# Optimization experiments

Measured on AMD Instinct MI355X. Metric: run time of the kernel, lower is better.

The kernel has to match this reference:

```python
import jax, jax.numpy as jnp
import numpy as np

N = 20000; E = 640000
D_IN = 1000; E1 = 500; E2 = 500; E3 = 2000; NZ = 10; NC = 10


def setup_inputs() -> dict:
    keys = iter(jax.random.split(jax.random.key(0), 80))

    def nrm(shape, s=0.05):
        return jax.random.normal(next(keys), shape, jnp.float32) * s

    inp = {"x": jax.random.normal(next(keys), (N, D_IN), jnp.float32)}
    for nm in ["adj", "fadj", "f1", "f2"]:
        inp[nm + "_rows"] = jax.random.randint(next(keys), (E,), 0, N, jnp.int32)
        inp[nm + "_cols"] = jax.random.randint(next(keys), (E,), 0, N, jnp.int32)
        inp[nm + "_vals"] = jax.random.uniform(next(keys), (E,), jnp.float32)
    dims = [D_IN, E1, E2, E3, NZ]
    for br in ["fea", "topo"]:
        for i in range(4):
            inp[br + "_W" + str(i + 1)] = nrm((dims[i], dims[i + 1]))
    ae_shapes = {"e1": (D_IN, E1), "e2": (E1, E2), "e3": (E2, E3), "z1": (E3, NZ),
                 "z2": (NZ, NC), "d0": (NC, NZ), "d1": (NZ, 2000), "d2": (2000, 500),
                 "d3": (500, 500), "xb": (500, D_IN)}
    for nm, sh in ae_shapes.items():
        inp["ae_W" + nm] = nrm(sh)
        inp["ae_b" + nm] = jnp.zeros((sh[1],), jnp.float32)
    inp["mlpL_W"] = nrm((3000 + NZ, 5))
    inp["mlpL_b"] = jnp.zeros((5,), jnp.float32)
    return inp


def _bn(h):
    # BatchNorm1d(affine=False, track_running_stats=False): batch stats, biased var
    return (h - h.mean(0)) * jax.lax.rsqrt(h.var(0) + 1e-5)


def _branch(x, rows, cols, vals, Ws):
    # stacked GNNLayer: dense mm -> spmm(adj, support) -> leaky_relu(0.2) -> elu -> BN
    hs = []
    h = x
    for W in Ws:
        sup = h @ W                                            # [N, out]
        agg = jax.ops.segment_sum(vals[:, None] * sup[cols], rows, num_segments=N)
        h = _bn(jax.nn.elu(jax.nn.leaky_relu(agg, 0.2)))
        hs.append(h)
    return hs


def _forward(x,
             adj_rows, adj_cols, adj_vals,
             fadj_rows, fadj_cols, fadj_vals,
             f1_rows, f1_cols, f1_vals,
             f2_rows, f2_cols, f2_vals,
             fea_W1, fea_W2, fea_W3, fea_W4,
             topo_W1, topo_W2, topo_W3, topo_W4,
             ae_We1, ae_be1, ae_We2, ae_be2, ae_We3, ae_be3,
             ae_Wz1, ae_bz1, ae_Wz2, ae_bz2,
             ae_Wd0, ae_bd0, ae_Wd1, ae_bd1, ae_Wd2, ae_bd2, ae_Wd3, ae_bd3,
             ae_Wxb, ae_bxb, mlpL_W, mlpL_b):
    relu = jax.nn.relu
    # AE branch
    h1 = relu(x @ ae_We1 + ae_be1)
    h2 = relu(h1 @ ae_We2 + ae_be2)
    h3 = relu(h2 @ ae_We3 + ae_be3)
    z1 = h3 @ ae_Wz1 + ae_bz1
    z = z1 @ ae_Wz2 + ae_bz2
    d = relu(z @ ae_Wd0 + ae_bd0)
    d = relu(d @ ae_Wd1 + ae_bd1)
    d = relu(d @ ae_Wd2 + ae_bd2)
    d = relu(d @ ae_Wd3 + ae_bd3)
    x_bar = d @ ae_Wxb + ae_bxb
    feaWs = [fea_W1, fea_W2, fea_W3, fea_W4]
    topoWs = [topo_W1, topo_W2, topo_W3, topo_W4]
    fea_hs = _branch(x, fadj_rows, fadj_cols, fadj_vals, feaWs)
    fea_diff = _branch(x, f2_rows, f2_cols, f2_vals, feaWs)
    topo_hs = _branch(x, adj_rows, adj_cols, adj_vals, topoWs)
    topo_diff = _branch(x, f1_rows, f1_cols, f1_vals, topoWs)
    coms = jnp.concatenate(fea_hs, axis=1)                      # [N, 3000+NZ]
    u = jax.nn.softmax(jnp.tanh(coms @ mlpL_W + mlpL_b), axis=1)
    u = u / jnp.maximum(jnp.linalg.norm(u, axis=1, keepdims=True), 1e-12)  # F.normalize p=2
    z_out_fea = jnp.concatenate([u[:, i:i + 1] * fea_hs[i] for i in range(4)], axis=1)
    return (x_bar, z, fea_hs[3], topo_hs[3], fea_diff[3], topo_diff[3], z_out_fea)


def reference(x,
              adj_rows, adj_cols, adj_vals,
              fadj_rows, fadj_cols, fadj_vals,
              f1_rows, f1_cols, f1_vals,
              f2_rows, f2_cols, f2_vals,
              fea_W1, fea_W2, fea_W3, fea_W4,
              topo_W1, topo_W2, topo_W3, topo_W4,
              ae_We1, ae_be1, ae_We2, ae_be2, ae_We3, ae_be3,
              ae_Wz1, ae_bz1, ae_Wz2, ae_bz2,
              ae_Wd0, ae_bd0, ae_Wd1, ae_bd1, ae_Wd2, ae_bd2, ae_Wd3, ae_bd3,
              ae_Wxb, ae_bxb, mlpL_W, mlpL_b):
    return _forward(x, adj_rows, adj_cols, adj_vals, fadj_rows, fadj_cols, fadj_vals,
                    f1_rows, f1_cols, f1_vals, f2_rows, f2_cols, f2_vals,
                    fea_W1, fea_W2, fea_W3, fea_W4, topo_W1, topo_W2, topo_W3, topo_W4,
                    ae_We1, ae_be1, ae_We2, ae_be2, ae_We3, ae_be3,
                    ae_Wz1, ae_bz1, ae_Wz2, ae_bz2,
                    ae_Wd0, ae_bd0, ae_Wd1, ae_bd1, ae_Wd2, ae_bd2, ae_Wd3, ae_bd3,
                    ae_Wxb, ae_bxb, mlpL_W, mlpL_b)
```

## Files before the change

### kernel.cpp

```cpp
#include <hip/hip_runtime.h>
#include <cstdint>
#include <cstddef>

#define N_NODES 20000
#define N_EDGES 640000

typedef short short8 __attribute__((ext_vector_type(8)));
typedef float floatx4 __attribute__((ext_vector_type(4)));

__device__ __forceinline__ ushort f2bf(float f) {
    uint32_t u = __float_as_uint(f);
    uint32_t r = (u + 0x7fff + ((u >> 16) & 1)) >> 16;
    return (ushort)r;
}
__device__ __forceinline__ float bf2f(ushort u) {
    return __uint_as_float(((uint32_t)u) << 16);
}

__global__ __launch_bounds__(256) void zero_i32(int* __restrict__ p, int n) {
    int i = blockIdx.x * 256 + threadIdx.x;
    if (i < n) p[i] = 0;
}

__global__ __launch_bounds__(256) void transpose_w(const float* __restrict__ W,
                                                   ushort* __restrict__ Bt,
                                                   int K, int Nc, int Kp) {
    int idx = blockIdx.x * 256 + threadIdx.x;
    if (idx >= Nc * Kp) return;
    int n = idx / Kp, k = idx % Kp;
    Bt[idx] = (k < K) ? f2bf(W[(size_t)k * Nc + n]) : (ushort)0;
}

__global__ __launch_bounds__(256) void hist_kernel(const int* __restrict__ rows,
                                                   int* __restrict__ counts) {
    int e = blockIdx.x * 256 + threadIdx.x;
    if (e < N_EDGES) atomicAdd(&counts[rows[e]], 1);
}

__global__ __launch_bounds__(1024) void scan_kernel(const int* __restrict__ counts,
                                                    int* __restrict__ row_ptr) {
    __shared__ int part[1024];
    const int CH = 20;
    int tid = threadIdx.x;
    int t0 = tid * CH;
    int s = 0;
    for (int i = 0; i < CH; ++i) {
        int p = t0 + i;
        if (p < N_NODES) s += counts[p];
    }
    part[tid] = s;
    __syncthreads();
    for (int off = 1; off < 1024; off <<= 1) {
        int v = (tid >= off) ? part[tid - off] : 0;
        __syncthreads();
        if (tid >= off) part[tid] += v;
        __syncthreads();
    }
    int base = (tid == 0) ? 0 : part[tid - 1];
    for (int i = 0; i < CH; ++i) {
        int p = t0 + i;
        if (p < N_NODES) {
            row_ptr[p] = base;
            base += counts[p];
            if (p == N_NODES - 1) row_ptr[N_NODES] = base;
        }
    }
}

__global__ __launch_bounds__(256) void fill_kernel(const int* __restrict__ rows,
                                                   const int* __restrict__ cols,
                                                   const float* __restrict__ vals,
                                                   const int* __restrict__ row_ptr,
                                                   int* __restrict__ fillctr,
                                                   int* __restrict__ cols_s,
                                                   float* __restrict__ vals_s) {
    int e = blockIdx.x * 256 + threadIdx.x;
    if (e < N_EDGES) {
        int r = rows[e];
        int pos = atomicAdd(&fillctr[r], 1);
        int idx = row_ptr[r] + pos;
        cols_s[idx] = cols[e];
        vals_s[idx] = vals[e];
    }
}

template <int AMODE>
__global__ __launch_bounds__(256) void mfma_gemm(
    const float* __restrict__ A, const ushort* __restrict__ Ab,
    const ushort* __restrict__ Bt,
    const float* __restrict__ bias, float* __restrict__ Cf,
    ushort* __restrict__ Cb, int M, int K, int lda, int Nc, int ldc, int Kp,
    int act, int NX, int NY) {
    __shared__ __align__(16) ushort As[128][40];
    __shared__ __align__(16) ushort Bs[128][40];
    __shared__ __align__(16) ushort Al[(AMODE == 1) ? 128 : 1][40];

    int id = blockIdx.x;
    int r8 = id & 7, tt = id >> 3;
    int bx = tt % NX, qq = tt / NX;
    int by = r8 + 8 * qq;
    if (by >= NY) return;
    int row0 = by * 128, col0 = bx * 128;

    int tid = threadIdx.x;
    int wave = tid >> 6, lane = tid & 63;
    int wr = (wave >> 1) * 64, wc = (wave & 1) * 64;
    int m16 = lane & 15, quad = lane >> 4;

    floatx4 acc[4][4] = {};
    int KT = (K + 31) >> 5;
    bool k4 = (K & 3) == 0;

    int arf = tid >> 3, akq = (tid & 7) << 2;
    int arb = tid >> 2, akb = (tid & 3) << 3;
    int bn_ = tid >> 2, bch = (tid & 3) << 3;

    float4 avA[4], avB[4];
    uint4 abvA[2], abvB[2], bvA[2], bvB[2];

#define ISSUE_T(AV, ABV, BV, KTARG)                                          \
    do {                                                                     \
        int k0_ = (KTARG) << 5;                                              \
        if constexpr (AMODE == 2) {                                          \
            for (int p = 0; p < 2; ++p) {                                    \
                int grow = row0 + arb + p * 64;                              \
                int gk = k0_ + akb;                                          \
                uint4 z = {0u, 0u, 0u, 0u};                                  \
                if (grow < M) {                                              \
                    const ushort* ap = Ab + (size_t)grow * lda + gk;         \
                    if (gk + 7 < K) {                                        \
                        z = *(const uint4*)ap;                               \
                    } else {                                                 \
                        ushort tm[8] = {0, 0, 0, 0, 0, 0, 0, 0};             \
                        for (int j = 0; j < 8; ++j)                          \
                            if (gk + j < K) tm[j] = ap[j];                   \
                        z.x = (uint)tm[0] | ((uint)tm[1] << 16);             \
                        z.y = (uint)tm[2] | ((uint)tm[3] << 16);             \
                        z.z = (uint)tm[4] | ((uint)tm[5] << 16);             \
                        z.w = (uint)tm[6] | ((uint)tm[7] << 16);             \
                    }                                                        \
                }                                                            \
                ABV[p] = z;                                                  \
            }                                                                \
        } else {                                                             \
            for (int p = 0; p < 4; ++p) {                                    \
                int grow = row0 + arf + p * 32;                              \
                int gk = k0_ + akq;                                          \
                float4 v = {0.f, 0.f, 0.f, 0.f};                             \
                if (grow < M) {                                              \
                    const float* ap = A + (size_t)grow * lda + gk;           \
                    if (k4 && gk + 3 < K) {                                  \
                        v = *(const float4*)ap;                              \
                    } else {                                                 \
                        if (gk < K) v.x = ap[0];                             \
                        if (gk + 1 < K) v.y = ap[1];                         \
                        if (gk + 2 < K) v.z = ap[2];                         \
                        if (gk + 3 < K) v.w = ap[3];                         \
                    }                                                        \
                }                                                            \
                AV[p] = v;                                                   \
            }                                                                \
        }                                                                    \
        for (int p = 0; p < 2; ++p) {                                        \
            int gcol = col0 + bn_ + p * 64;                                  \
            uint4 z = {0u, 0u, 0u, 0u};                                      \
            if (gcol < Nc) z = *(const uint4*)&Bt[(size_t)gcol * Kp + k0_ + bch]; \
            BV[p] = z;                                                       \
        }                                                                    \
    } while (0)

#define WRITE_T(AV, ABV, BV)                                                 \
    do {                                                                     \
        if constexpr (AMODE == 2) {                                          \
            for (int p = 0; p < 2; ++p)                                      \
                *(uint4*)&As[arb + p * 64][akb] = ABV[p];                    \
        } else {                                                             \
            for (int p = 0; p < 4; ++p) {                                    \
                float4 v = AV[p];                                            \
                ushort4 hi;                                                  \
                hi.x = f2bf(v.x); hi.y = f2bf(v.y);                          \
                hi.z = f2bf(v.z); hi.w = f2bf(v.w);                          \
                *(ushort4*)&As[arf + p * 32][akq] = hi;                      \
                if constexpr (AMODE == 1) {                                  \
                    ushort4 lo;                                              \
                    lo.x = f2bf(v.x - bf2f(hi.x));                           \
                    lo.y = f2bf(v.y - bf2f(hi.y));                           \
                    lo.z = f2bf(v.z - bf2f(hi.z));                           \
                    lo.w = f2bf(v.w - bf2f(hi.w));                           \
                    *(ushort4*)&Al[arf + p * 32][akq] = lo;                  \
                }                                                            \
            }                                                                \
        }                                                                    \
        for (int p = 0; p < 2; ++p)                                          \
            *(uint4*)&Bs[bn_ + p * 64][bch] = BV[p];                         \
    } while (0)

    ISSUE_T(avA, abvA, bvA, 0);
    for (int kt = 0; kt < KT; ++kt) {
        if (kt) __syncthreads();
        if ((kt & 1) == 0) {
            WRITE_T(avA, abvA, bvA);
            if (kt + 1 < KT) ISSUE_T(avB, abvB, bvB, kt + 1);
        } else {
            WRITE_T(avB, abvB, bvB);
            if (kt + 1 < KT) ISSUE_T(avA, abvA, bvA, kt + 1);
        }
        __syncthreads();
        short8 a[4], b[4];
        int ko = quad * 8;
#pragma unroll
        for (int i = 0; i < 4; ++i) a[i] = *(short8*)&As[wr + i * 16 + m16][ko];
#pragma unroll
        for (int j = 0; j < 4; ++j) b[j] = *(short8*)&Bs[wc + j * 16 + m16][ko];
        if constexpr (AMODE == 1) {
            short8 al[4];
#pragma unroll
            for (int i = 0; i < 4; ++i) al[i] = *(short8*)&Al[wr + i * 16 + m16][ko];
#pragma unroll
            for (int i = 0; i < 4; ++i)
#pragma unroll
                for (int j = 0; j < 4; ++j)
                    acc[i][j] = __builtin_amdgcn_mfma_f32_16x16x32_bf16(
                        al[i], b[j], acc[i][j], 0, 0, 0);
        }
#pragma unroll
        for (int i = 0; i < 4; ++i)
#pragma unroll
            for (int j = 0; j < 4; ++j)
                acc[i][j] = __builtin_amdgcn_mfma_f32_16x16x32_bf16(
                    a[i], b[j], acc[i][j], 0, 0, 0);
    }
#undef ISSUE_T
#undef WRITE_T

#pragma unroll
    for (int i = 0; i < 4; ++i) {
        int rbase = row0 + wr + i * 16 + quad * 4;
#pragma unroll
        for (int j = 0; j < 4; ++j) {
            int gcol = col0 + wc + j * 16 + m16;
            if (gcol >= Nc) continue;
            float bv = bias ? bias[gcol] : 0.f;
#pragma unroll
            for (int r = 0; r < 4; ++r) {
                int grow = rbase + r;
                if (grow >= M) continue;
                float v = acc[i][j][r] + bv;
                if (act == 1) v = v > 0.f ? v : 0.f;
                else if (act == 2) v = v > 0.f ? v : (expf(0.2f * v) - 1.0f);
                if (Cb) Cb[(size_t)grow * ldc + gcol] = f2bf(v);
                else Cf[(size_t)grow * ldc + gcol] = v;
            }
        }
    }
}

__global__ __launch_bounds__(256) void gemm_small(
    const float* __restrict__ A, const float* __restrict__ B,
    const float* __restrict__ bias, float* __restrict__ C,
    int M, int K, int Nc, int act) {
    int row = blockIdx.x * 8 + (threadIdx.x >> 5);
    int c = threadIdx.x & 31;
    if (row >= M || c >= Nc) return;
    float acc = bias ? bias[c] : 0.f;
    for (int k = 0; k < K; ++k) acc += A[(size_t)row * K + k] * B[(size_t)k * Nc + c];
    if (act) acc = acc > 0.f ? acc : 0.f;
    C[(size_t)row * Nc + c] = acc;
}


template <int ACT, int OUTBF>
__global__ __launch_bounds__(128) void spmm_f32in(
    const float* __restrict__ sup, const int* __restrict__ rp,
    const int* __restrict__ cols_s, const float* __restrict__ vals_s,
    float* __restrict__ outf, ushort* __restrict__ outb,
    int C, int ldin, int ldout) {
    int r = blockIdx.x;
    int f0 = (blockIdx.y * 128 + threadIdx.x) * 4;
    if (f0 >= C) return;
    int s = rp[r], e = rp[r + 1];
    const float* sb = sup + f0;
    floatx4 A0 = {0.f, 0.f, 0.f, 0.f}, A1 = A0, A2 = A0, A3 = A0;
    int i = s;
    for (; i + 4 <= e; i += 4) {
        int c0 = cols_s[i], c1 = cols_s[i + 1], c2 = cols_s[i + 2],
            c3 = cols_s[i + 3];
        float v0 = vals_s[i], v1 = vals_s[i + 1], v2 = vals_s[i + 2],
              v3 = vals_s[i + 3];
        floatx4 u0 = *(const floatx4*)(sb + (size_t)c0 * ldin);
        floatx4 u1 = *(const floatx4*)(sb + (size_t)c1 * ldin);
        floatx4 u2 = *(const floatx4*)(sb + (size_t)c2 * ldin);
        floatx4 u3 = *(const floatx4*)(sb + (size_t)c3 * ldin);
        A0 += v0 * u0;
        A1 += v1 * u1;
        A2 += v2 * u2;
        A3 += v3 * u3;
    }
    int n = e - i;
    if (n > 0) {
        int c0 = cols_s[i];
        int c1 = cols_s[i + (n > 1 ? 1 : 0)];
        int c2 = cols_s[i + (n > 2 ? 2 : 0)];
        float v0 = vals_s[i];
        float v1 = n > 1 ? vals_s[i + 1] : 0.f;
        float v2 = n > 2 ? vals_s[i + 2] : 0.f;
        floatx4 u0 = *(const floatx4*)(sb + (size_t)c0 * ldin);
        floatx4 u1 = *(const floatx4*)(sb + (size_t)c1 * ldin);
        floatx4 u2 = *(const floatx4*)(sb + (size_t)c2 * ldin);
        A0 += v0 * u0;
        A1 += v1 * u1;
        A2 += v2 * u2;
    }
    floatx4 acc = (A0 + A1) + (A2 + A3);
    if (ACT) {
#pragma unroll
        for (int k = 0; k < 4; ++k)
            acc[k] = acc[k] > 0.f ? acc[k] : (expf(0.2f * acc[k]) - 1.0f);
    }
    if (OUTBF) {
        ushort4 w;
        w.x = f2bf(acc[0]); w.y = f2bf(acc[1]);
        w.z = f2bf(acc[2]); w.w = f2bf(acc[3]);
        *(ushort4*)&outb[(size_t)r * ldout + f0] = w;
    } else {
        *(floatx4*)&outf[(size_t)r * ldout + f0] = acc;
    }
}

template <int ACT, int OUTF32>
__global__ __launch_bounds__(128) void spmm_bf16in(
    const ushort* __restrict__ sup, const int* __restrict__ rp,
    const int* __restrict__ cols_s, const float* __restrict__ vals_s,
    float* __restrict__ outf, ushort* __restrict__ outb,
    int C, int ldin, int ldout) {
    int r = blockIdx.x;
    int f0 = (blockIdx.y * 128 + threadIdx.x) * 4;
    if (f0 >= C) return;
    int s = rp[r], e = rp[r + 1];
    const ushort* sb = sup + f0;
    floatx4 A0 = {0.f, 0.f, 0.f, 0.f}, A1 = A0, A2 = A0, A3 = A0;
    int i = s;
#define UNPK(ACCV, VV, QQ)                                                   \
    do {                                                                     \
        ACCV[0] += VV * bf2f((ushort)(QQ.x & 0xffff));                       \
        ACCV[1] += VV * bf2f((ushort)(QQ.x >> 16));                          \
        ACCV[2] += VV * bf2f((ushort)(QQ.y & 0xffff));                       \
        ACCV[3] += VV * bf2f((ushort)(QQ.y >> 16));                          \
    } while (0)
    for (; i + 4 <= e; i += 4) {
        int c0 = cols_s[i], c1 = cols_s[i + 1], c2 = cols_s[i + 2],
            c3 = cols_s[i + 3];
        float v0 = vals_s[i], v1 = vals_s[i + 1], v2 = vals_s[i + 2],
              v3 = vals_s[i + 3];
        uint2 q0 = *(const uint2*)(sb + (size_t)c0 * ldin);
        uint2 q1 = *(const uint2*)(sb + (size_t)c1 * ldin);
        uint2 q2 = *(const uint2*)(sb + (size_t)c2 * ldin);
        uint2 q3 = *(const uint2*)(sb + (size_t)c3 * ldin);
        UNPK(A0, v0, q0);
        UNPK(A1, v1, q1);
        UNPK(A2, v2, q2);
        UNPK(A3, v3, q3);
    }
    int n = e - i;
    if (n > 0) {
        int c0 = cols_s[i];
        int c1 = cols_s[i + (n > 1 ? 1 : 0)];
        int c2 = cols_s[i + (n > 2 ? 2 : 0)];
        float v0 = vals_s[i];
        float v1 = n > 1 ? vals_s[i + 1] : 0.f;
        float v2 = n > 2 ? vals_s[i + 2] : 0.f;
        uint2 q0 = *(const uint2*)(sb + (size_t)c0 * ldin);
        uint2 q1 = *(const uint2*)(sb + (size_t)c1 * ldin);
        uint2 q2 = *(const uint2*)(sb + (size_t)c2 * ldin);
        UNPK(A0, v0, q0);
        UNPK(A1, v1, q1);
        UNPK(A2, v2, q2);
    }
#undef UNPK
    floatx4 acc = (A0 + A1) + (A2 + A3);
    if (ACT) {
#pragma unroll
        for (int k = 0; k < 4; ++k)
            acc[k] = acc[k] > 0.f ? acc[k] : (expf(0.2f * acc[k]) - 1.0f);
    }
    if (OUTF32) {
        *(floatx4*)&outf[(size_t)r * ldout + f0] = acc;
    } else {
        ushort4 w;
        w.x = f2bf(acc[0]); w.y = f2bf(acc[1]);
        w.z = f2bf(acc[2]); w.w = f2bf(acc[3]);
        *(ushort4*)&outb[(size_t)r * ldout + f0] = w;
    }
}

__global__ __launch_bounds__(256) void spmm_small_bf(
    const ushort* __restrict__ sup, const int* __restrict__ rp,
    const int* __restrict__ cols_s, const float* __restrict__ vals_s,
    ushort* __restrict__ t, int C, int ldin) {
    __shared__ float red[16][17];
    int r = blockIdx.x;
    int f = threadIdx.x & 15, sub = threadIdx.x >> 4;
    int s = rp[r], e = rp[r + 1];
    float acc = 0.f;
    if (f < C) {
        for (int i = s + sub; i < e; i += 16)
            acc += vals_s[i] * bf2f(sup[(size_t)cols_s[i] * ldin + f]);
    }
    red[sub][f] = acc;
    __syncthreads();
    if (sub == 0 && f < C) {
        float a = 0.f;
#pragma unroll
        for (int k = 0; k < 16; ++k) a += red[k][f];
        float o = a > 0.f ? a : (expf(0.2f * a) - 1.0f);
        t[(size_t)r * C + f] = f2bf(o);
    }
}

__global__ __launch_bounds__(256) void spmm_small_f(
    const float* __restrict__ sup, const int* __restrict__ rp,
    const int* __restrict__ cols_s, const float* __restrict__ vals_s,
    float* __restrict__ t, int C, int ldin) {
    __shared__ float red[16][17];
    int r = blockIdx.x;
    int f = threadIdx.x & 15, sub = threadIdx.x >> 4;
    int s = rp[r], e = rp[r + 1];
    float acc = 0.f;
    if (f < C) {
        for (int i = s + sub; i < e; i += 16)
            acc += vals_s[i] * sup[(size_t)cols_s[i] * ldin + f];
    }
    red[sub][f] = acc;
    __syncthreads();
    if (sub == 0 && f < C) {
        float a = 0.f;
#pragma unroll
        for (int k = 0; k < 16; ++k) a += red[k][f];
        t[(size_t)r * C + f] = a > 0.f ? a : (expf(0.2f * a) - 1.0f);
    }
}

__global__ __launch_bounds__(256) void col_stats(const ushort* __restrict__ t,
                                                 float* __restrict__ sum,
                                                 float* __restrict__ sumsq, int C,
                                                 int rpb) {
    int c = blockIdx.x * 256 + threadIdx.x;
    int r0 = blockIdx.y * rpb;
    if (c >= C) return;
    float s = 0.f, ss = 0.f;
    for (int r = r0; r < r0 + rpb; ++r) {
        float v = bf2f(t[(size_t)r * C + c]);
        s += v;
        ss += v * v;
    }
    atomicAdd(&sum[c], s);
    atomicAdd(&sumsq[c], ss);
}

__global__ __launch_bounds__(256) void bn_apply(const ushort* __restrict__ t,
                                                const float* __restrict__ sum,
                                                const float* __restrict__ sumsq,
                                                float* __restrict__ h, int C) {
    int c = blockIdx.x * 256 + threadIdx.x;
    int r = blockIdx.y;
    if (c >= C) return;
    float mean = sum[c] * (1.0f / N_NODES);
    float var = sumsq[c] * (1.0f / N_NODES) - mean * mean;
    float rs = rsqrtf(var + 1e-5f);
    h[(size_t)r * C + c] = (bf2f(t[(size_t)r * C + c]) - mean) * rs;
}

__global__ __launch_bounds__(256) void bn_apply_bb(const ushort* __restrict__ t,
                                                   const float* __restrict__ sum,
                                                   const float* __restrict__ sumsq,
                                                   ushort* __restrict__ h, int C,
                                                   int ldh) {
    int c = blockIdx.x * 256 + threadIdx.x;
    int r = blockIdx.y;
    if (c >= C) return;
    float mean = sum[c] * (1.0f / N_NODES);
    float var = sumsq[c] * (1.0f / N_NODES) - mean * mean;
    float rs = rsqrtf(var + 1e-5f);
    h[(size_t)r * ldh + c] = f2bf((bf2f(t[(size_t)r * C + c]) - mean) * rs);
}

__global__ __launch_bounds__(256) void bn_elem_bf(const ushort* __restrict__ t,
                                                  const float* __restrict__ sum,
                                                  const float* __restrict__ sumsq,
                                                  float* __restrict__ h, int C,
                                                  int total) {
    int idx = blockIdx.x * 256 + threadIdx.x;
    if (idx >= total) return;
    int c = idx % C;
    float mean = sum[c] * (1.0f / N_NODES);
    float var = sumsq[c] * (1.0f / N_NODES) - mean * mean;
    float rs = rsqrtf(var + 1e-5f);
    h[idx] = (bf2f(t[idx]) - mean) * rs;
}

__global__ __launch_bounds__(256) void bn_elem_f(float* __restrict__ t,
                                                 const float* __restrict__ sum,
                                                 const float* __restrict__ sumsq,
                                                 int C, int total) {
    int idx = blockIdx.x * 256 + threadIdx.x;
    if (idx >= total) return;
    int c = idx % C;
    float mean = sum[c] * (1.0f / N_NODES);
    float var = sumsq[c] * (1.0f / N_NODES) - mean * mean;
    float rs = rsqrtf(var + 1e-5f);
    t[idx] = (t[idx] - mean) * rs;
}

__global__ __launch_bounds__(256) void col_stats_f(const float* __restrict__ t,
                                                   float* __restrict__ sum,
                                                   float* __restrict__ sumsq, int C,
                                                   int rpb) {
    int c = blockIdx.x * 256 + threadIdx.x;
    int r0 = blockIdx.y * rpb;
    if (c >= C) return;
    float s = 0.f, ss = 0.f;
    for (int r = r0; r < r0 + rpb; ++r) {
        float v = t[(size_t)r * C + c];
        s += v;
        ss += v * v;
    }
    atomicAdd(&sum[c], s);
    atomicAdd(&sumsq[c], ss);
}

__global__ __launch_bounds__(256) void bn_apply_f(const float* __restrict__ t,
                                                  const float* __restrict__ sum,
                                                  const float* __restrict__ sumsq,
                                                  float* __restrict__ h, int C) {
    int c = blockIdx.x * 256 + threadIdx.x;
    int r = blockIdx.y;
    if (c >= C) return;
    float mean = sum[c] * (1.0f / N_NODES);
    float var = sumsq[c] * (1.0f / N_NODES) - mean * mean;
    float rs = rsqrtf(var + 1e-5f);
    h[(size_t)r * C + c] = (t[(size_t)r * C + c] - mean) * rs;
}

__global__ __launch_bounds__(256) void mlp_u(const float* __restrict__ h1,
                                             const float* __restrict__ h2,
                                             const float* __restrict__ h3,
                                             const float* __restrict__ h4,
                                             const float* __restrict__ W,
                                             const float* __restrict__ b,
                                             float* __restrict__ u) {
    int lane = threadIdx.x & 63;
    int wv = threadIdx.x >> 6;
    int row = blockIdx.x * 4 + wv;
    if (row >= N_NODES) return;
    float acc[5] = {0.f, 0.f, 0.f, 0.f, 0.f};
    const float* hs[4] = {h1, h2, h3, h4};
    const int Cs[4] = {500, 500, 2000, 10};
    const int Woff[4] = {0, 500, 1000, 3000};
    for (int sg = 0; sg < 4; ++sg) {
        const float* hp = hs[sg] + (size_t)row * Cs[sg];
        const float* wp = W + (size_t)Woff[sg] * 5;
        for (int k = lane; k < Cs[sg]; k += 64) {
            float a = hp[k];
#pragma unroll
            for (int j = 0; j < 5; ++j) acc[j] += a * wp[k * 5 + j];
        }
    }
#pragma unroll
    for (int j = 0; j < 5; ++j)
        for (int off = 32; off > 0; off >>= 1) acc[j] += __shfl_down(acc[j], off, 64);
    if (lane == 0) {
        float t[5], m = -1e30f;
#pragma unroll
        for (int j = 0; j < 5; ++j) {
            t[j] = tanhf(acc[j] + b[j]);
            m = fmaxf(m, t[j]);
        }
        float s = 0.f;
#pragma unroll
        for (int j = 0; j < 5; ++j) {
            t[j] = expf(t[j] - m);
            s += t[j];
        }
        float inv = 1.0f / s;
        float n2 = 0.f;
#pragma unroll
        for (int j = 0; j < 5; ++j) {
            t[j] *= inv;
            n2 += t[j] * t[j];
        }
        float nrm = fmaxf(sqrtf(n2), 1e-12f);
        float innrm = 1.0f / nrm;
#pragma unroll
        for (int j = 0; j < 5; ++j) u[(size_t)row * 5 + j] = t[j] * innrm;
    }
}

__global__ __launch_bounds__(256) void zout_kernel(const float* __restrict__ h1,
                                                   const float* __restrict__ h2,
                                                   const float* __restrict__ h3,
                                                   const float* __restrict__ h4,
                                                   const float* __restrict__ u,
                                                   float* __restrict__ out) {
    int c = blockIdx.x * 256 + threadIdx.x;
    int row = blockIdx.y;
    if (c >= 3010) return;
    int seg, cl;
    const float* hp;
    if (c < 500)       { seg = 0; cl = c;        hp = h1 + (size_t)row * 500; }
    else if (c < 1000) { seg = 1; cl = c - 500;  hp = h2 + (size_t)row * 500; }
    else if (c < 3000) { seg = 2; cl = c - 1000; hp = h3 + (size_t)row * 2000; }
    else               { seg = 3; cl = c - 3000; hp = h4 + (size_t)row * 10; }
    out[(size_t)row * 3010 + c] = u[(size_t)row * 5 + seg] * hp[cl];
}

extern "C" void kernel_launch(void* const* d_in, const int* in_sizes, int n_in,
                              void* d_out, int out_size, void* d_ws, size_t ws_size,
                              hipStream_t stream) {
    const float* x = (const float*)d_in[0];
    const int* adj_rows  = (const int*)d_in[1];
    const int* adj_cols  = (const int*)d_in[2];
    const float* adj_vals = (const float*)d_in[3];
    const int* fadj_rows = (const int*)d_in[4];
    const int* fadj_cols = (const int*)d_in[5];
    const float* fadj_vals = (const float*)d_in[6];
    const int* f1_rows = (const int*)d_in[7];
    const int* f1_cols = (const int*)d_in[8];
    const float* f1_vals = (const float*)d_in[9];
    const int* f2_rows = (const int*)d_in[10];
    const int* f2_cols = (const int*)d_in[11];
    const float* f2_vals = (const float*)d_in[12];
    const float* feaW[4]  = {(const float*)d_in[13], (const float*)d_in[14],
                             (const float*)d_in[15], (const float*)d_in[16]};
    const float* topoW[4] = {(const float*)d_in[17], (const float*)d_in[18],
                             (const float*)d_in[19], (const float*)d_in[20]};
    const float* We1 = (const float*)d_in[21]; const float* be1 = (const float*)d_in[22];
    const float* We2 = (const float*)d_in[23]; const float* be2 = (const float*)d_in[24];
    const float* We3 = (const float*)d_in[25]; const float* be3 = (const float*)d_in[26];
    const float* Wz1 = (const float*)d_in[27]; const float* bz1 = (const float*)d_in[28];
    const float* Wz2 = (const float*)d_in[29]; const float* bz2 = (const float*)d_in[30];
    const float* Wd0 = (const float*)d_in[31]; const float* bd0 = (const float*)d_in[32];
    const float* Wd1 = (const float*)d_in[33]; const float* bd1 = (const float*)d_in[34];
    const float* Wd2 = (const float*)d_in[35]; const float* bd2 = (const float*)d_in[36];
    const float* Wd3 = (const float*)d_in[37]; const float* bd3 = (const float*)d_in[38];
    const float* Wxb = (const float*)d_in[39]; const float* bxb = (const float*)d_in[40];
    const float* mlpW = (const float*)d_in[41]; const float* mlpb = (const float*)d_in[42];

    float* out = (float*)d_out;
    float* out_xbar = out;
    float* out_z = out + 20000000;
    float* out_fea4 = out + 20200000;
    float* out_topo4 = out + 20400000;
    float* out_feadiff4 = out + 20600000;
    float* out_topodiff4 = out + 20800000;
    float* out_zout = out + 21000000;

    char* w = (char*)d_ws;
    auto alloc = [&](size_t bytes) -> char* {
        char* p = w;
        w += (bytes + 255) & ~(size_t)255;
        return p;
    };
    ushort* bufB = (ushort*)alloc((size_t)N_NODES * 2000 * 2);
    ushort* bufC = (ushort*)alloc((size_t)N_NODES * 2000 * 2);
    float* feah1 = (float*)alloc((size_t)N_NODES * 500 * 4);
    float* feah2 = (float*)alloc((size_t)N_NODES * 500 * 4);
    float* feah3 = (float*)alloc((size_t)N_NODES * 2000 * 4);
    float* bufH  = (float*)alloc((size_t)N_NODES * 2000 * 4);
    ushort* bufHb = (ushort*)(bufH + 10000000);
    float* supFea = bufH + 30000000;
    float* z1buf = (float*)alloc((size_t)N_NODES * 10 * 4);
    float* dsmall = (float*)alloc((size_t)N_NODES * 10 * 4);
    float* ubuf  = (float*)alloc((size_t)N_NODES * 5 * 4);
    float* ssum  = (float*)alloc(2000 * 4);
    float* ssq   = (float*)alloc(2000 * 4);
    int* counts  = (int*)alloc(N_NODES * 4);
    int* fillctr = (int*)alloc(N_NODES * 4);
    int* row_ptr = (int*)alloc((N_NODES + 1) * 4);
    int* cols_s  = (int*)alloc((size_t)N_EDGES * 4);
    float* vals_s = (float*)alloc((size_t)N_EDGES * 4);
    ushort* supTopo = (ushort*)alloc((size_t)N_NODES * 500 * 2);

    ushort* aeh1b = bufC;
    ushort* aeh2b = bufC + (size_t)N_NODES * 512;
    ushort* aeh3b = bufB;

    auto kpad = [](int K) { return ((K + 31) / 32) * 32; };
    struct TW { const float* W; int K, Nc, Kp; ushort* Bt; };
    TW tw[16] = {
        {We1, 1000, 500, 1024, nullptr}, {We2, 500, 500, 512, nullptr},
        {We3, 500, 2000, 512, nullptr},  {Wz1, 2000, 10, 2016, nullptr},
        {Wd1, 10, 2000, 32, nullptr},    {Wd2, 2000, 500, 2016, nullptr},
        {Wd3, 500, 500, 512, nullptr},   {Wxb, 500, 1000, 512, nullptr},
        {feaW[0], 1000, 500, 1024, nullptr}, {feaW[1], 500, 500, 512, nullptr},
        {feaW[2], 500, 2000, 512, nullptr},  {feaW[3], 2000, 10, 2016, nullptr},
        {topoW[0], 1000, 500, 1024, nullptr}, {topoW[1], 500, 500, 512, nullptr},
        {topoW[2], 500, 2000, 512, nullptr},  {topoW[3], 2000, 10, 2016, nullptr},
    };
    for (int i = 0; i < 16; ++i) {
        tw[i].Kp = kpad(tw[i].K);
        tw[i].Bt = (ushort*)alloc((size_t)tw[i].Nc * tw[i].Kp * 2);
        int tot = tw[i].Nc * tw[i].Kp;
        transpose_w<<<(tot + 255) / 256, 256, 0, stream>>>(
            tw[i].W, tw[i].Bt, tw[i].K, tw[i].Nc, tw[i].Kp);
    }

    const int NYB = (N_NODES + 127) / 128;
    const int NY8 = 8 * ((NYB + 7) / 8);
    auto gemm_f32 = [&](const float* A, const TW& t, const float* bias, float* Cf,
                        ushort* Cb, int lda, int ldc, int act) {
        int NX = (t.Nc + 127) / 128;
        mfma_gemm<0><<<NX * NY8, 256, 0, stream>>>(A, nullptr, t.Bt, bias, Cf, Cb,
                                                   N_NODES, t.K, lda, t.Nc, ldc,
                                                   t.Kp, act, NX, NYB);
    };
    auto gemm_spl = [&](const float* A, const TW& t, float* Cf, int lda, int ldc,
                        int act) {
        int NX = (t.Nc + 127) / 128;
        mfma_gemm<1><<<NX * NY8, 256, 0, stream>>>(A, nullptr, t.Bt, nullptr, Cf,
                                                   nullptr, N_NODES, t.K, lda, t.Nc,
                                                   ldc, t.Kp, act, NX, NYB);
    };
    auto gemm_b16 = [&](const ushort* Ab, const TW& t, const float* bias, float* Cf,
                        ushort* Cb, int lda, int ldc, int act) {
        int NX = (t.Nc + 127) / 128;
        mfma_gemm<2><<<NX * NY8, 256, 0, stream>>>(nullptr, Ab, t.Bt, bias, Cf, Cb,
                                                   N_NODES, t.K, lda, t.Nc, ldc,
                                                   t.Kp, act, NX, NYB);
    };

    gemm_f32(x, tw[0], be1, nullptr, aeh1b, 1000, 512, 1);
    gemm_b16(aeh1b, tw[1], be2, nullptr, aeh2b, 512, 512, 1);
    gemm_b16(aeh2b, tw[2], be3, nullptr, aeh3b, 512, 2000, 1);
    gemm_b16(aeh3b, tw[3], bz1, z1buf, nullptr, 2000, 10, 0);
    gemm_small<<<(N_NODES + 7) / 8, 256, 0, stream>>>(z1buf, Wz2, bz2, out_z,
                                                      N_NODES, 10, 10, 0);
    gemm_small<<<(N_NODES + 7) / 8, 256, 0, stream>>>(out_z, Wd0, bd0, dsmall,
                                                      N_NODES, 10, 10, 1);
    gemm_f32(dsmall, tw[4], bd1, nullptr, aeh3b, 10, 2000, 1);
    gemm_b16(aeh3b, tw[5], bd2, nullptr, aeh1b, 2000, 512, 1);
    gemm_b16(aeh1b, tw[6], bd3, nullptr, aeh2b, 512, 512, 1);
    gemm_b16(aeh2b, tw[7], bxb, out_xbar, nullptr, 512, 1000, 0);

    gemm_f32(x, tw[12], nullptr, nullptr, supTopo, 1000, 500, 0);

    struct Br {
        const int* rows; const int* cols; const float* vals;
        int w0;
        float* final_dest;
    };
    Br brs[4] = {
        {fadj_rows, fadj_cols, fadj_vals, 8, out_fea4},
        {adj_rows, adj_cols, adj_vals, 12, out_topo4},
        {f2_rows, f2_cols, f2_vals, 8, out_feadiff4},
        {f1_rows, f1_cols, f1_vals, 12, out_topodiff4},
    };

    auto bn_zero = [&](int C) {
        zero_i32<<<(C + 255) / 256, 256, 0, stream>>>((int*)ssum, C);
        zero_i32<<<(C + 255) / 256, 256, 0, stream>>>((int*)ssq, C);
    };
    auto bn_f = [&](float* t, int C) {
        bn_zero(C);
        if (C <= 16) {
            col_stats_f<<<dim3(1, 200), 256, 0, stream>>>(t, ssum, ssq, C, 100);
            int tot = N_NODES * C;
            bn_elem_f<<<(tot + 255) / 256, 256, 0, stream>>>(t, ssum, ssq, C, tot);
        } else {
            col_stats_f<<<dim3((C + 255) / 256, 100), 256, 0, stream>>>(
                t, ssum, ssq, C, 200);
            bn_apply_f<<<dim3((C + 255) / 256, N_NODES), 256, 0, stream>>>(
                t, ssum, ssq, t, C);
        }
    };
    auto bn_bb = [&](const ushort* t, ushort* h, int C, int ldh) {
        bn_zero(C);
        col_stats<<<dim3((C + 255) / 256, 100), 256, 0, stream>>>(t, ssum, ssq, C,
                                                                  200);
        bn_apply_bb<<<dim3((C + 255) / 256, N_NODES), 256, 0, stream>>>(
            t, ssum, ssq, h, C, ldh);
    };
    auto bn_bf_small = [&](const ushort* t, float* h, int C) {
        bn_zero(C);
        col_stats<<<dim3(1, 200), 256, 0, stream>>>(t, ssum, ssq, C, 100);
        int tot = N_NODES * C;
        bn_elem_bf<<<(tot + 255) / 256, 256, 0, stream>>>(t, ssum, ssq, h, C, tot);
    };

    for (int b = 0; b < 4; ++b) {
        zero_i32<<<(N_NODES + 255) / 256, 256, 0, stream>>>(counts, N_NODES);
        hist_kernel<<<(N_EDGES + 255) / 256, 256, 0, stream>>>(brs[b].rows, counts);
        scan_kernel<<<1, 1024, 0, stream>>>(counts, row_ptr);
        zero_i32<<<(N_NODES + 255) / 256, 256, 0, stream>>>(fillctr, N_NODES);
        fill_kernel<<<(N_EDGES + 255) / 256, 256, 0, stream>>>(
            brs[b].rows, brs[b].cols, brs[b].vals, row_ptr, fillctr, cols_s, vals_s);

        int w0 = brs[b].w0;
        if (b == 0) {
            gemm_spl(x, tw[w0], supFea, 1000, 500, 0);
            spmm_f32in<1, 0><<<dim3(N_NODES, 1), 128, 0, stream>>>(
                supFea, row_ptr, cols_s, vals_s, feah1, nullptr, 500, 500, 500);
            bn_f(feah1, 500);
            gemm_spl(feah1, tw[w0 + 1], bufH, 500, 500, 0);
            spmm_f32in<1, 0><<<dim3(N_NODES, 1), 128, 0, stream>>>(
                bufH, row_ptr, cols_s, vals_s, feah2, nullptr, 500, 500, 500);
            bn_f(feah2, 500);
            spmm_f32in<0, 0><<<dim3(N_NODES, 1), 128, 0, stream>>>(
                feah2, row_ptr, cols_s, vals_s, bufH, nullptr, 500, 500, 500);
            gemm_spl(bufH, tw[w0 + 2], feah3, 500, 2000, 2);
            bn_f(feah3, 2000);
            gemm_spl(feah3, tw[w0 + 3], bufH, 2000, 10, 0);
            spmm_small_f<<<N_NODES, 256, 0, stream>>>(bufH, row_ptr, cols_s, vals_s,
                                                      brs[b].final_dest, 10, 10);
            bn_f(brs[b].final_dest, 10);
        } else {
            if (b == 2) {
                spmm_f32in<1, 1><<<dim3(N_NODES, 1), 128, 0, stream>>>(
                    supFea, row_ptr, cols_s, vals_s, nullptr, bufC, 500, 500, 500);
            } else {
                spmm_bf16in<1, 0><<<dim3(N_NODES, 1), 128, 0, stream>>>(
                    supTopo, row_ptr, cols_s, vals_s, nullptr, bufC, 500, 500, 500);
            }
            bn_bb(bufC, bufHb, 500, 512);
            gemm_b16(bufHb, tw[w0 + 1], nullptr, nullptr, bufB, 512, 500, 0);
            spmm_bf16in<1, 0><<<dim3(N_NODES, 1), 128, 0, stream>>>(
                bufB, row_ptr, cols_s, vals_s, nullptr, bufC, 500, 500, 500);
            bn_bb(bufC, bufHb, 500, 512);
            spmm_bf16in<0, 1><<<dim3(N_NODES, 1), 128, 0, stream>>>(
                bufHb, row_ptr, cols_s, vals_s, bufH, nullptr, 500, 512, 500);
            gemm_f32(bufH, tw[w0 + 2], nullptr, nullptr, bufC, 500, 2000, 2);
            bn_bb(bufC, bufHb, 2000, 2000);
            gemm_b16(bufHb, tw[w0 + 3], nullptr, nullptr, bufB, 2000, 10, 0);
            spmm_small_bf<<<N_NODES, 256, 0, stream>>>(bufB, row_ptr, cols_s, vals_s,
                                                       bufC, 10, 10);
            bn_bf_small(bufC, brs[b].final_dest, 10);
        }
    }

    mlp_u<<<(N_NODES + 3) / 4, 256, 0, stream>>>(feah1, feah2, feah3, out_fea4,
                                                 mlpW, mlpb, ubuf);
    zout_kernel<<<dim3(12, N_NODES), 256, 0, stream>>>(feah1, feah2, feah3, out_fea4,
                                                       ubuf, out_zout);
}
```

Measured before the change: 5.690 ms.

## Fold batchnorm into following GEMM weights and pre-split fp32 inputs into bf16 hi/lo

For the bf16 branches, the separate batchnorm apply pass is removed. Per-column reciprocal std is folded into a rescaled transposed weight, and the mean term is folded into a GEMM bias, or into the SpMM through a running sum of edge values. For the fp32 branch, activations are split once into bf16 hi/lo buffers, either inside BN-apply and SpMM epilogues or in a split kernel, so a new GEMM mode 3 loads them directly instead of converting inside the GEMM. This drops several full N×C read/write passes, at the cost of extra small per-call weight-scaling and bias kernels and some loss of precision in the folded path.

```diff
diff --git a/kernel.cpp b/kernel.cpp
--- a/kernel.cpp
+++ b/kernel.cpp
@@ -29,6 +29,53 @@
     if (idx >= Nc * Kp) return;
     int n = idx / Kp, k = idx % Kp;
     Bt[idx] = (k < K) ? f2bf(W[(size_t)k * Nc + n]) : (ushort)0;
+}
+
+__global__ __launch_bounds__(256) void scale_bt(const float* __restrict__ W,
+                                                const float* __restrict__ rs,
+                                                ushort* __restrict__ Bt,
+                                                int K, int Nc, int Kp) {
+    int idx = blockIdx.x * 256 + threadIdx.x;
+    if (idx >= Nc * Kp) return;
+    int n = idx / Kp, k = idx % Kp;
+    Bt[idx] = (k < K) ? f2bf(rs[k] * W[(size_t)k * Nc + n]) : (ushort)0;
+}
+
+__global__ __launch_bounds__(256) void fold_bias(const float* __restrict__ W,
+                                                 const float* __restrict__ mean,
+                                                 const float* __restrict__ rs,
+                                                 float* __restrict__ bias,
+                                                 int K, int Nc) {
+    int n = blockIdx.x * 256 + threadIdx.x;
+    if (n >= Nc) return;
+    float s = 0.f;
+    for (int k = 0; k < K; ++k) s += mean[k] * rs[k] * W[(size_t)k * Nc + n];
+    bias[n] = -s;
+}
+
+__global__ __launch_bounds__(256) void finalize_stats(const float* __restrict__ ssum,
+                                                      const float* __restrict__ ssq,
+                                                      float* __restrict__ mean,
+                                                      float* __restrict__ rs, int C) {
+    int c = blockIdx.x * 256 + threadIdx.x;
+    if (c >= C) return;
+    float m = ssum[c] * (1.0f / N_NODES);
+    float var = ssq[c] * (1.0f / N_NODES) - m * m;
+    mean[c] = m;
+    rs[c] = rsqrtf(var + 1e-5f);
+}
+
+__global__ __launch_bounds__(256) void split_f32(const float* __restrict__ A,
+                                                 ushort* __restrict__ hi,
+                                                 ushort* __restrict__ lo,
+                                                 int M, int K, int ldo) {
+    int idx = blockIdx.x * 256 + threadIdx.x;
+    if (idx >= M * ldo) return;
+    int r = idx / ldo, k = idx % ldo;
+    float v = (k < K) ? A[(size_t)r * K + k] : 0.f;
+    ushort h = f2bf(v);
+    hi[idx] = h;
+    lo[idx] = f2bf(v - bf2f(h));
 }
 
 __global__ __launch_bounds__(256) void hist_kernel(const int* __restrict__ rows,
@@ -87,13 +134,13 @@
 template <int AMODE>
 __global__ __launch_bounds__(256) void mfma_gemm(
     const float* __restrict__ A, const ushort* __restrict__ Ab,
-    const ushort* __restrict__ Bt,
+    const ushort* __restrict__ Abl, const ushort* __restrict__ Bt,
     const float* __restrict__ bias, float* __restrict__ Cf,
     ushort* __restrict__ Cb, int M, int K, int lda, int Nc, int ldc, int Kp,
     int act, int NX, int NY) {
     __shared__ __align__(16) ushort As[128][40];
     __shared__ __align__(16) ushort Bs[128][40];
-    __shared__ __align__(16) ushort Al[(AMODE == 1) ? 128 : 1][40];
+    __shared__ __align__(16) ushort Al[(AMODE == 1 || AMODE == 3) ? 128 : 1][40];
 
     int id = blockIdx.x;
     int r8 = id & 7, tt = id >> 3;
@@ -116,32 +163,38 @@
     int bn_ = tid >> 2, bch = (tid & 3) << 3;
 
     float4 avA[4], avB[4];
-    uint4 abvA[2], abvB[2], bvA[2], bvB[2];
-
-#define ISSUE_T(AV, ABV, BV, KTARG)                                          \
+    uint4 abvA[2], abvB[2], albA[2], albB[2], bvA[2], bvB[2];
+
+#define LOAD_B16(DST, BASE, K0_)                                             \
+    do {                                                                     \
+        for (int p = 0; p < 2; ++p) {                                        \
+            int grow = row0 + arb + p * 64;                                  \
+            int gk = (K0_) + akb;                                            \
+            uint4 z = {0u, 0u, 0u, 0u};                                      \
+            if (grow < M) {                                                  \
+                const ushort* ap = (BASE) + (size_t)grow * lda + gk;         \
+                if (gk + 7 < K) {                                            \
+                    z = *(const uint4*)ap;                                   \
+                } else {                                                     \
+                    ushort tm[8] = {0, 0, 0, 0, 0, 0, 0, 0};                 \
+                    for (int j = 0; j < 8; ++j)                              \
+                        if (gk + j < K) tm[j] = ap[j];                       \
+                    z.x = (uint)tm[0] | ((uint)tm[1] << 16);                 \
+                    z.y = (uint)tm[2] | ((uint)tm[3] << 16);                 \
+                    z.z = (uint)tm[4] | ((uint)tm[5] << 16);                 \
+                    z.w = (uint)tm[6] | ((uint)tm[7] << 16);                 \
+                }                                                            \
+            }                                                                \
+            DST[p] = z;                                                      \
+        }                                                                    \
+    } while (0)
+
+#define ISSUE_T(AV, ABV, ALB, BV, KTARG)                                     \
     do {                                                                     \
         int k0_ = (KTARG) << 5;                                              \
-        if constexpr (AMODE == 2) {                                          \
-            for (int p = 0; p < 2; ++p) {                                    \
-                int grow = row0 + arb + p * 64;                              \
-                int gk = k0_ + akb;                                          \
-                uint4 z = {0u, 0u, 0u, 0u};                                  \
-                if (grow < M) {                                              \
-                    const ushort* ap = Ab + (size_t)grow * lda + gk;         \
-                    if (gk + 7 < K) {                                        \
-                        z = *(const uint4*)ap;                               \
-                    } else {                                                 \
-                        ushort tm[8] = {0, 0, 0, 0, 0, 0, 0, 0};             \
-                        for (int j = 0; j < 8; ++j)                          \
-                            if (gk + j < K) tm[j] = ap[j];                   \
-                        z.x = (uint)tm[0] | ((uint)tm[1] << 16);             \
-                        z.y = (uint)tm[2] | ((uint)tm[3] << 16);             \
-                        z.z = (uint)tm[4] | ((uint)tm[5] << 16);             \
-                        z.w = (uint)tm[6] | ((uint)tm[7] << 16);             \
-                    }                                                        \
-                }                                                            \
-                ABV[p] = z;                                                  \
-            }                                                                \
+        if constexpr (AMODE >= 2) {                                          \
+            LOAD_B16(ABV, Ab, k0_);                                          \
+            if constexpr (AMODE == 3) LOAD_B16(ALB, Abl, k0_);               \
         } else {                                                             \
             for (int p = 0; p < 4; ++p) {                                    \
                 int grow = row0 + arf + p * 32;                              \
@@ -169,11 +222,14 @@
         }                                                                    \
     } while (0)
 
-#define WRITE_T(AV, ABV, BV)                                                 \
+#define WRITE_T(AV, ABV, ALB, BV)                                            \
     do {                                                                     \
-        if constexpr (AMODE == 2) {                                          \
+        if constexpr (AMODE >= 2) {                                          \
             for (int p = 0; p < 2; ++p)                                      \
                 *(uint4*)&As[arb + p * 64][akb] = ABV[p];                    \
+            if constexpr (AMODE == 3)                                        \
+                for (int p = 0; p < 2; ++p)                                  \
+                    *(uint4*)&Al[arb + p * 64][akb] = ALB[p];                \
         } else {                                                             \
             for (int p = 0; p < 4; ++p) {                                    \
                 float4 v = AV[p];                                            \
@@ -195,15 +251,15 @@
             *(uint4*)&Bs[bn_ + p * 64][bch] = BV[p];                         \
     } while (0)
 
-    ISSUE_T(avA, abvA, bvA, 0);
+    ISSUE_T(avA, abvA, albA, bvA, 0);
     for (int kt = 0; kt < KT; ++kt) {
         if (kt) __syncthreads();
         if ((kt & 1) == 0) {
-            WRITE_T(avA, abvA, bvA);
-            if (kt + 1 < KT) ISSUE_T(avB, abvB, bvB, kt + 1);
+            WRITE_T(avA, abvA, albA, bvA);
+            if (kt + 1 < KT) ISSUE_T(avB, abvB, albB, bvB, kt + 1);
         } else {
-            WRITE_T(avB, abvB, bvB);
-            if (kt + 1 < KT) ISSUE_T(avA, abvA, bvA, kt + 1);
+            WRITE_T(avB, abvB, albB, bvB);
+            if (kt + 1 < KT) ISSUE_T(avA, abvA, albA, bvA, kt + 1);
         }
         __syncthreads();
         short8 a[4], b[4];
@@ -212,7 +268,7 @@
         for (int i = 0; i < 4; ++i) a[i] = *(short8*)&As[wr + i * 16 + m16][ko];
 #pragma unroll
         for (int j = 0; j < 4; ++j) b[j] = *(short8*)&Bs[wc + j * 16 + m16][ko];
-        if constexpr (AMODE == 1) {
+        if constexpr (AMODE == 1 || AMODE == 3) {
             short8 al[4];
 #pragma unroll
             for (int i = 0; i < 4; ++i) al[i] = *(short8*)&Al[wr + i * 16 + m16][ko];
@@ -232,6 +288,7 @@
     }
 #undef ISSUE_T
 #undef WRITE_T
+#undef LOAD_B16
 
 #pragma unroll
     for (int i = 0; i < 4; ++i) {
@@ -268,13 +325,12 @@
     C[(size_t)row * Nc + c] = acc;
 }
 
-
-template <int ACT, int OUTBF>
+template <int ACT, int OUTMODE>
 __global__ __launch_bounds__(128) void spmm_f32in(
     const float* __restrict__ sup, const int* __restrict__ rp,
     const int* __restrict__ cols_s, const float* __restrict__ vals_s,
     float* __restrict__ outf, ushort* __restrict__ outb,
-    int C, int ldin, int ldout) {
+    ushort* __restrict__ outb2, int C, int ldin, int ldout) {
     int r = blockIdx.x;
     int f0 = (blockIdx.y * 128 + threadIdx.x) * 4;
     if (f0 >= C) return;
@@ -317,28 +373,39 @@
         for (int k = 0; k < 4; ++k)
             acc[k] = acc[k] > 0.f ? acc[k] : (expf(0.2f * acc[k]) - 1.0f);
     }
-    if (OUTBF) {
+    if (OUTMODE == 0) {
+        *(floatx4*)&outf[(size_t)r * ldout + f0] = acc;
+    } else if (OUTMODE == 1) {
         ushort4 w;
         w.x = f2bf(acc[0]); w.y = f2bf(acc[1]);
         w.z = f2bf(acc[2]); w.w = f2bf(acc[3]);
         *(ushort4*)&outb[(size_t)r * ldout + f0] = w;
     } else {
-        *(floatx4*)&outf[(size_t)r * ldout + f0] = acc;
-    }
-}
-
-template <int ACT, int OUTF32>
+        ushort4 h, l;
+#pragma unroll
+        for (int k = 0; k < 4; ++k) {
+            ushort hb = f2bf(acc[k]);
+            ((ushort*)&h)[k] = hb;
+            ((ushort*)&l)[k] = f2bf(acc[k] - bf2f(hb));
+        }
+        *(ushort4*)&outb[(size_t)r * ldout + f0] = h;
+        *(ushort4*)&outb2[(size_t)r * ldout + f0] = l;
+    }
+}
+
+template <int MODE>
 __global__ __launch_bounds__(128) void spmm_bf16in(
     const ushort* __restrict__ sup, const int* __restrict__ rp,
     const int* __restrict__ cols_s, const float* __restrict__ vals_s,
-    float* __restrict__ outf, ushort* __restrict__ outb,
-    int C, int ldin, int ldout) {
+    ushort* __restrict__ outb, const float* __restrict__ mean,
+    const float* __restrict__ rs, int C, int ldin, int ldout) {
     int r = blockIdx.x;
     int f0 = (blockIdx.y * 128 + threadIdx.x) * 4;
     if (f0 >= C) return;
     int s = rp[r], e = rp[r + 1];
     const ushort* sb = sup + f0;
     floatx4 A0 = {0.f, 0.f, 0.f, 0.f}, A1 = A0, A2 = A0, A3 = A0;
+    float vsum = 0.f;
     int i = s;
 #define UNPK(ACCV, VV, QQ)                                                   \
     do {                                                                     \
@@ -360,6 +427,7 @@
         UNPK(A1, v1, q1);
         UNPK(A2, v2, q2);
         UNPK(A3, v3, q3);
+        if (MODE == 1) vsum += v0 + v1 + v2 + v3;
     }
     int n = e - i;
     if (n > 0) {
@@ -375,22 +443,23 @@
         UNPK(A0, v0, q0);
         UNPK(A1, v1, q1);
         UNPK(A2, v2, q2);
+        if (MODE == 1) vsum += v0 + v1 + v2;
     }
 #undef UNPK
     floatx4 acc = (A0 + A1) + (A2 + A3);
-    if (ACT) {
+    if (MODE == 0) {
 #pragma unroll
         for (int k = 0; k < 4; ++k)
             acc[k] = acc[k] > 0.f ? acc[k] : (expf(0.2f * acc[k]) - 1.0f);
-    }
-    if (OUTF32) {
-        *(floatx4*)&outf[(size_t)r * ldout + f0] = acc;
     } else {
-        ushort4 w;
-        w.x = f2bf(acc[0]); w.y = f2bf(acc[1]);
-        w.z = f2bf(acc[2]); w.w = f2bf(acc[3]);
-        *(ushort4*)&outb[(size_t)r * ldout + f0] = w;
-    }
+#pragma unroll
+        for (int k = 0; k < 4; ++k)
+            acc[k] = rs[f0 + k] * (acc[k] - mean[f0 + k] * vsum);
+    }
+    ushort4 w;
+    w.x = f2bf(acc[0]); w.y = f2bf(acc[1]);
+    w.z = f2bf(acc[2]); w.w = f2bf(acc[3]);
+    *(ushort4*)&outb[(size_t)r * ldout + f0] = w;
 }
 
 __global__ __launch_bounds__(256) void spmm_small_bf(
@@ -443,13 +512,13 @@
 __global__ __launch_bounds__(256) void col_stats(const ushort* __restrict__ t,
                                                  float* __restrict__ sum,
                                                  float* __restrict__ sumsq, int C,
-                                                 int rpb) {
+                                                 int rpb, int ld) {
     int c = blockIdx.x * 256 + threadIdx.x;
     int r0 = blockIdx.y * rpb;
     if (c >= C) return;
     float s = 0.f, ss = 0.f;
     for (int r = r0; r < r0 + rpb; ++r) {
-        float v = bf2f(t[(size_t)r * C + c]);
+        float v = bf2f(t[(size_t)r * ld + c]);
         s += v;
         ss += v * v;
     }
@@ -457,31 +526,51 @@
     atomicAdd(&sumsq[c], ss);
 }
 
-__global__ __launch_bounds__(256) void bn_apply(const ushort* __restrict__ t,
-                                                const float* __restrict__ sum,
-                                                const float* __restrict__ sumsq,
-                                                float* __restrict__ h, int C) {
+__global__ __launch_bounds__(256) void col_stats_f(const float* __restrict__ t,
+                                                   float* __restrict__ sum,
+                                                   float* __restrict__ sumsq, int C,
+                                                   int rpb) {
+    int c = blockIdx.x * 256 + threadIdx.x;
+    int r0 = blockIdx.y * rpb;
+    if (c >= C) return;
+    float s = 0.f, ss = 0.f;
+    for (int r = r0; r < r0 + rpb; ++r) {
+        float v = t[(size_t)r * C + c];
+        s += v;
+        ss += v * v;
+    }
+    atomicAdd(&sum[c], s);
+    atomicAdd(&sumsq[c], ss);
+}
+
+__global__ __launch_bounds__(256) void bn_apply_f(const float* __restrict__ t,
+                                                  const float* __restrict__ sum,
+                                                  const float* __restrict__ sumsq,
+                                                  float* __restrict__ h, int C) {
     int c = blockIdx.x * 256 + threadIdx.x;
     int r = blockIdx.y;
     if (c >= C) return;
     float mean = sum[c] * (1.0f / N_NODES);
     float var = sumsq[c] * (1.0f / N_NODES) - mean * mean;
     float rs = rsqrtf(var + 1e-5f);
-    h[(size_t)r * C + c] = (bf2f(t[(size_t)r * C + c]) - mean) * rs;
-}
-
-__global__ __launch_bounds__(256) void bn_apply_bb(const ushort* __restrict__ t,
-                                                   const float* __restrict__ sum,
-                                                   const float* __restrict__ sumsq,
-                                                   ushort* __restrict__ h, int C,
-                                                   int ldh) {
+    h[(size_t)r * C + c] = (t[(size_t)r * C + c] - mean) * rs;
+}
+
+__global__ __launch_bounds__(256) void bn_apply_f_split(
+    const float* __restrict__ t, const float* __restrict__ sum,
+    const float* __restrict__ sumsq, float* __restrict__ h,
+    ushort* __restrict__ hi, ushort* __restrict__ lo, int C, int ldh) {
     int c = blockIdx.x * 256 + threadIdx.x;
     int r = blockIdx.y;
     if (c >= C) return;
     float mean = sum[c] * (1.0f / N_NODES);
     float var = sumsq[c] * (1.0f / N_NODES) - mean * mean;
     float rs = rsqrtf(var + 1e-5f);
-    h[(size_t)r * ldh + c] = f2bf((bf2f(t[(size_t)r * C + c]) - mean) * rs);
+    float v = (t[(size_t)r * C + c] - mean) * rs;
+    h[(size_t)r * C + c] = v;
+    ushort hb = f2bf(v);
+    hi[(size_t)r * ldh + c] = hb;
+    lo[(size_t)r * ldh + c] = f2bf(v - bf2f(hb));
 }
 
 __global__ __launch_bounds__(256) void bn_elem_bf(const ushort* __restrict__ t,
@@ -509,36 +598,6 @@
     float var = sumsq[c] * (1.0f / N_NODES) - mean * mean;
     float rs = rsqrtf(var + 1e-5f);
     t[idx] = (t[idx] - mean) * rs;
-}
-
-__global__ __launch_bounds__(256) void col_stats_f(const float* __restrict__ t,
-                                                   float* __restrict__ sum,
-                                                   float* __restrict__ sumsq, int C,
-                                                   int rpb) {
-    int c = blockIdx.x * 256 + threadIdx.x;
-    int r0 = blockIdx.y * rpb;
-    if (c >= C) return;
-    float s = 0.f, ss = 0.f;
-    for (int r = r0; r < r0 + rpb; ++r) {
-        float v = t[(size_t)r * C + c];
-        s += v;
-        ss += v * v;
-    }
-    atomicAdd(&sum[c], s);
-    atomicAdd(&sumsq[c], ss);
-}
-
-__global__ __launch_bounds__(256) void bn_apply_f(const float* __restrict__ t,
-                                                  const float* __restrict__ sum,
-                                                  const float* __restrict__ sumsq,
-                                                  float* __restrict__ h, int C) {
-    int c = blockIdx.x * 256 + threadIdx.x;
-    int r = blockIdx.y;
-    if (c >= C) return;
-    float mean = sum[c] * (1.0f / N_NODES);
-    float var = sumsq[c] * (1.0f / N_NODES) - mean * mean;
-    float rs = rsqrtf(var + 1e-5f);
-    h[(size_t)r * C + c] = (t[(size_t)r * C + c] - mean) * rs;
 }
 
 __global__ __launch_bounds__(256) void mlp_u(const float* __restrict__ h1,
@@ -660,19 +719,30 @@
         w += (bytes + 255) & ~(size_t)255;
         return p;
     };
-    ushort* bufB = (ushort*)alloc((size_t)N_NODES * 2000 * 2);
-    ushort* bufC = (ushort*)alloc((size_t)N_NODES * 2000 * 2);
+    ushort* bufB = (ushort*)alloc((size_t)N_NODES * 2048 * 2);
+    ushort* bufC = (ushort*)alloc((size_t)N_NODES * 2048 * 2);
     float* feah1 = (float*)alloc((size_t)N_NODES * 500 * 4);
     float* feah2 = (float*)alloc((size_t)N_NODES * 500 * 4);
     float* feah3 = (float*)alloc((size_t)N_NODES * 2000 * 4);
+    ushort* xhi = (ushort*)feah3;
+    ushort* xlo = xhi + (size_t)N_NODES * 1024;
+    ushort* h1hi = xlo + (size_t)N_NODES * 1024;
+    ushort* h1lo = h1hi + (size_t)N_NODES * 512;
     float* bufH  = (float*)alloc((size_t)N_NODES * 2000 * 4);
     ushort* bufHb = (ushort*)(bufH + 10000000);
+    ushort* ghi = bufHb;
+    ushort* glo = bufHb + (size_t)N_NODES * 512;
     float* supFea = bufH + 30000000;
     float* z1buf = (float*)alloc((size_t)N_NODES * 10 * 4);
     float* dsmall = (float*)alloc((size_t)N_NODES * 10 * 4);
     float* ubuf  = (float*)alloc((size_t)N_NODES * 5 * 4);
     float* ssum  = (float*)alloc(2000 * 4);
     float* ssq   = (float*)alloc(2000 * 4);
+    float* meanb = (float*)alloc(2000 * 4);
+    float* rsb   = (float*)alloc(2000 * 4);
+    float* biasS = (float*)alloc(2000 * 4);
+    ushort* btS1 = (ushort*)alloc((size_t)500 * 512 * 2);
+    ushort* btS3 = (ushort*)alloc((size_t)10 * 2016 * 2);
     int* counts  = (int*)alloc(N_NODES * 4);
     int* fillctr = (int*)alloc(N_NODES * 4);
     int* row_ptr = (int*)alloc((N_NODES + 1) * 4);
@@ -706,42 +776,59 @@
 
     const int NYB = (N_NODES + 127) / 128;
     const int NY8 = 8 * ((NYB + 7) / 8);
-    auto gemm_f32 = [&](const float* A, const TW& t, const float* bias, float* Cf,
-                        ushort* Cb, int lda, int ldc, int act) {
-        int NX = (t.Nc + 127) / 128;
-        mfma_gemm<0><<<NX * NY8, 256, 0, stream>>>(A, nullptr, t.Bt, bias, Cf, Cb,
-                                                   N_NODES, t.K, lda, t.Nc, ldc,
-                                                   t.Kp, act, NX, NYB);
+    auto launch_gemm = [&](int amode, const float* A, const ushort* Ah,
+                           const ushort* Alo, const ushort* Bt, int K, int Nc,
+                           int Kp, const float* bias, float* Cf, ushort* Cb,
+                           int lda, int ldc, int act) {
+        int NX = (Nc + 127) / 128;
+        dim3 g(NX * NY8);
+        if (amode == 0)
+            mfma_gemm<0><<<g, 256, 0, stream>>>(A, nullptr, nullptr, Bt, bias, Cf,
+                                                Cb, N_NODES, K, lda, Nc, ldc, Kp,
+                                                act, NX, NYB);
+        else if (amode == 1)
+            mfma_gemm<1><<<g, 256, 0, stream>>>(A, nullptr, nullptr, Bt, bias, Cf,
+                                                Cb, N_NODES, K, lda, Nc, ldc, Kp,
+                                                act, NX, NYB);
+        else if (amode == 2)
+            mfma_gemm<2><<<g, 256, 0, stream>>>(nullptr, Ah, nullptr, Bt, bias, Cf,
+                                                Cb, N_NODES, K, lda, Nc, ldc, Kp,
+                                                act, NX, NYB);
+        else
+            mfma_gemm<3><<<g, 256, 0, stream>>>(nullptr, Ah, Alo, Bt, bias, Cf,
+                                                Cb, N_NODES, K, lda, Nc, ldc, Kp,
+                                                act, NX, NYB);
     };
-    auto gemm_spl = [&](const float* A, const TW& t, float* Cf, int lda, int ldc,
-                        int act) {
-        int NX = (t.Nc + 127) / 128;
-        mfma_gemm<1><<<NX * NY8, 256, 0, stream>>>(A, nullptr, t.Bt, nullptr, Cf,
-                                                   nullptr, N_NODES, t.K, lda, t.Nc,
-                                                   ldc, t.Kp, act, NX, NYB);
-    };
-    auto gemm_b16 = [&](const ushort* Ab, const TW& t, const float* bias, float* Cf,
-                        ushort* Cb, int lda, int ldc, int act) {
-        int NX = (t.Nc + 127) / 128;
-        mfma_gemm<2><<<NX * NY8, 256, 0, stream>>>(nullptr, Ab, t.Bt, bias, Cf, Cb,
-                                                   N_NODES, t.K, lda, t.Nc, ldc,
-                                                   t.Kp, act, NX, NYB);
-    };
-
-    gemm_f32(x, tw[0], be1, nullptr, aeh1b, 1000, 512, 1);
-    gemm_b16(aeh1b, tw[1], be2, nullptr, aeh2b, 512, 512, 1);
-    gemm_b16(aeh2b, tw[2], be3, nullptr, aeh3b, 512, 2000, 1);
-    gemm_b16(aeh3b, tw[3], bz1, z1buf, nullptr, 2000, 10, 0);
+
+    {
+        int tot = N_NODES * 1024;
+        split_f32<<<(tot + 255) / 256, 256, 0, stream>>>(x, xhi, xlo, N_NODES,
+                                                         1000, 1024);
+    }
+
+    launch_gemm(2, nullptr, xhi, nullptr, tw[0].Bt, 1000, 500, 1024, be1, nullptr,
+                aeh1b, 1024, 512, 1);
+    launch_gemm(2, nullptr, aeh1b, nullptr, tw[1].Bt, 500, 500, 512, be2, nullptr,
+                aeh2b, 512, 512, 1);
+    launch_gemm(2, nullptr, aeh2b, nullptr, tw[2].Bt, 500, 2000, 512, be3, nullptr,
+                aeh3b, 512, 2000, 1);
+    launch_gemm(2, nullptr, aeh3b, nullptr, tw[3].Bt, 2000, 10, 2016, bz1, z1buf,
+                nullptr, 2000, 10, 0);
     gemm_small<<<(N_NODES + 7) / 8, 256, 0, stream>>>(z1buf, Wz2, bz2, out_z,
                                                       N_NODES, 10, 10, 0);
     gemm_small<<<(N_NODES + 7) / 8, 256, 0, stream>>>(out_z, Wd0, bd0, dsmall,
                                                       N_NODES, 10, 10, 1);
-    gemm_f32(dsmall, tw[4], bd1, nullptr, aeh3b, 10, 2000, 1);
-    gemm_b16(aeh3b, tw[5], bd2, nullptr, aeh1b, 2000, 512, 1);
-    gemm_b16(aeh1b, tw[6], bd3, nullptr, aeh2b, 512, 512, 1);
-    gemm_b16(aeh2b, tw[7], bxb, out_xbar, nullptr, 512, 1000, 0);
-
-    gemm_f32(x, tw[12], nullptr, nullptr, supTopo, 1000, 500, 0);
+    launch_gemm(0, dsmall, nullptr, nullptr, tw[4].Bt, 10, 2000, 32, bd1, nullptr,
+                aeh3b, 10, 2000, 1);
+    launch_gemm(2, nullptr, aeh3b, nullptr, tw[5].Bt, 2000, 500, 2016, bd2, nullptr,
+                aeh1b, 2000, 512, 1);
+    launch_gemm(2, nullptr, aeh1b, nullptr, tw[6].Bt, 500, 500, 512, bd3, nullptr,
+                aeh2b, 512, 512, 1);
+    launch_gemm(2, nullptr, aeh2b, nullptr, tw[7].Bt, 500, 1000, 512, bxb, out_xbar,
+                nullptr, 512, 1000, 0);
+
+    launch_gemm(2, nullptr, xhi, nullptr, tw[12].Bt, 1000, 500, 1024, nullptr,
+                nullptr, supTopo, 1024, 500, 0);
 
     struct Br {
         const int* rows; const int* cols; const float* vals;
@@ -758,6 +845,13 @@
     auto bn_zero = [&](int C) {
         zero_i32<<<(C + 255) / 256, 256, 0, stream>>>((int*)ssum, C);
         zero_i32<<<(C + 255) / 256, 256, 0, stream>>>((int*)ssq, C);
+    };
+    auto stats_bf = [&](const ushort* t, int C, int ld) {
+        bn_zero(C);
+        col_stats<<<dim3((C + 255) / 256, 100), 256, 0, stream>>>(t, ssum, ssq, C,
+                                                                  200, ld);
+        finalize_stats<<<(C + 255) / 256, 256, 0, stream>>>(ssum, ssq, meanb, rsb,
+                                                            C);
     };
     auto bn_f = [&](float* t, int C) {
         bn_zero(C);
@@ -772,19 +866,6 @@
                 t, ssum, ssq, t, C);
         }
     };
-    auto bn_bb = [&](const ushort* t, ushort* h, int C, int ldh) {
-        bn_zero(C);
-        col_stats<<<dim3((C + 255) / 256, 100), 256, 0, stream>>>(t, ssum, ssq, C,
-                                                                  200);
-        bn_apply_bb<<<dim3((C + 255) / 256, N_NODES), 256, 0, stream>>>(
-            t, ssum, ssq, h, C, ldh);
-    };
-    auto bn_bf_small = [&](const ushort* t, float* h, int C) {
-        bn_zero(C);
-        col_stats<<<dim3(1, 200), 256, 0, stream>>>(t, ssum, ssq, C, 100);
-        int tot = N_NODES * C;
-        bn_elem_bf<<<(tot + 255) / 256, 256, 0, stream>>>(t, ssum, ssq, h, C, tot);
-    };
 
     for (int b = 0; b < 4; ++b) {
         zero_i32<<<(N_NODES + 255) / 256, 256, 0, stream>>>(counts, N_NODES);
@@ -796,43 +877,78 @@
 
         int w0 = brs[b].w0;
         if (b == 0) {
-            gemm_spl(x, tw[w0], supFea, 1000, 500, 0);
+            launch_gemm(3, nullptr, xhi, xlo, tw[w0].Bt, 1000, 500, 1024, nullptr,
+                        supFea, nullptr, 1024, 500, 0);
             spmm_f32in<1, 0><<<dim3(N_NODES, 1), 128, 0, stream>>>(
-                supFea, row_ptr, cols_s, vals_s, feah1, nullptr, 500, 500, 500);
-            bn_f(feah1, 500);
-            gemm_spl(feah1, tw[w0 + 1], bufH, 500, 500, 0);
+                supFea, row_ptr, cols_s, vals_s, feah1, nullptr, nullptr, 500, 500,
+                500);
+            bn_zero(500);
+            col_stats_f<<<dim3(2, 100), 256, 0, stream>>>(feah1, ssum, ssq, 500,
+                                                          200);
+            bn_apply_f_split<<<dim3(2, N_NODES), 256, 0, stream>>>(
+                feah1, ssum, ssq, feah1, h1hi, h1lo, 500, 512);
+            launch_gemm(3, nullptr, h1hi, h1lo, tw[w0 + 1].Bt, 500, 500, 512,
+                        nullptr, bufH, nullptr, 512, 500, 0);
             spmm_f32in<1, 0><<<dim3(N_NODES, 1), 128, 0, stream>>>(
-                bufH, row_ptr, cols_s, vals_s, feah2, nullptr, 500, 500, 500);
+                bufH, row_ptr, cols_s, vals_s, feah2, nullptr, nullptr, 500, 500,
+                500);
             bn_f(feah2, 500);
-            spmm_f32in<0, 0><<<dim3(N_NODES, 1), 128, 0, stream>>>(
-                feah2, row_ptr, cols_s, vals_s, bufH, nullptr, 500, 500, 500);
-            gemm_spl(bufH, tw[w0 + 2], feah3, 500, 2000, 2);
+            spmm_f32in<0, 2><<<dim3(N_NODES, 1), 128, 0, stream>>>(
+                feah2, row_ptr, cols_s, vals_s, nullptr, ghi, glo, 500, 500, 512);
+            launch_gemm(3, nullptr, ghi, glo, tw[w0 + 2].Bt, 500, 2000, 512,
+                        nullptr, feah3, nullptr, 512, 2000, 2);
             bn_f(feah3, 2000);
-            gemm_spl(feah3, tw[w0 + 3], bufH, 2000, 10, 0);
+            launch_gemm(1, feah3, nullptr, nullptr, tw[w0 + 3].Bt, 2000, 10, 2016,
+                        nullptr, bufH, nullptr, 2000, 10, 0);
             spmm_small_f<<<N_NODES, 256, 0, stream>>>(bufH, row_ptr, cols_s, vals_s,
                                                       brs[b].final_dest, 10, 10);
             bn_f(brs[b].final_dest, 10);
         } else {
             if (b == 2) {
                 spmm_f32in<1, 1><<<dim3(N_NODES, 1), 128, 0, stream>>>(
-                    supFea, row_ptr, cols_s, vals_s, nullptr, bufC, 500, 500, 500);
+                    supFea, row_ptr, cols_s, vals_s, nullptr, bufC, nullptr, 500,
+                    500, 512);
             } else {
-                spmm_bf16in<1, 0><<<dim3(N_NODES, 1), 128, 0, stream>>>(
-                    supTopo, row_ptr, cols_s, vals_s, nullptr, bufC, 500, 500, 500);
+                spmm_bf16in<0><<<dim3(N_NODES, 1), 128, 0, stream>>>(
+                    supTopo, row_ptr, cols_s, vals_s, bufC, nullptr, nullptr, 500,
+                    500, 512);
             }
-            bn_bb(bufC, bufHb, 500, 512);
-            gemm_b16(bufHb, tw[w0 + 1], nullptr, nullptr, bufB, 512, 500, 0);
-            spmm_bf16in<1, 0><<<dim3(N_NODES, 1), 128, 0, stream>>>(
-                bufB, row_ptr, cols_s, vals_s, nullptr, bufC, 500, 500, 500);
-            bn_bb(bufC, bufHb, 500, 512);
-            spmm_bf16in<0, 1><<<dim3(N_NODES, 1), 128, 0, stream>>>(
-                bufHb, row_ptr, cols_s, vals_s, bufH, nullptr, 500, 512, 500);
-            gemm_f32(bufH, tw[w0 + 2], nullptr, nullptr, bufC, 500, 2000, 2);
-            bn_bb(bufC, bufHb, 2000, 2000);
-            gemm_b16(bufHb, tw[w0 + 3], nullptr, nullptr, bufB, 2000, 10, 0);
-            spmm_small_bf<<<N_NODES, 256, 0, stream>>>(bufB, row_ptr, cols_s, vals_s,
-                                                       bufC, 10, 10);
-            bn_bf_small(bufC, brs[b].final_dest, 10);
+            stats_bf(bufC, 500, 512);
+            {
+                const float* W2 = brs[b].w0 == 8 ? feaW[1] : topoW[1];
+                int tot = 500 * 512;
+                scale_bt<<<(tot + 255) / 256, 256, 0, stream>>>(W2, rsb, btS1, 500,
+                                                                500, 512);
+                fold_bias<<<2, 256, 0, stream>>>(W2, meanb, rsb, biasS, 500, 500);
+            }
+            launch_gemm(2, nullptr, bufC, nullptr, btS1, 500, 500, 512, biasS,
+                        nullptr, bufB, 512, 512, 0);
+            spmm_bf16in<0><<<dim3(N_NODES, 1), 128, 0, stream>>>(
+                bufB, row_ptr, cols_s, vals_s, bufC, nullptr, nullptr, 500, 512,
+                512);
+            stats_bf(bufC, 500, 512);
+            spmm_bf16in<1><<<dim3(N_NODES, 1), 128, 0, stream>>>(
+                bufC, row_ptr, cols_s, vals_s, bufHb, meanb, rsb, 500, 512, 512);
+            launch_gemm(2, nullptr, bufHb, nullptr, tw[w0 + 2].Bt, 500, 2000, 512,
+                        nullptr, nullptr, bufC, 512, 2048, 2);
+            stats_bf(bufC, 2000, 2048);
+            {
+                const float* W4 = brs[b].w0 == 8 ? feaW[3] : topoW[3];
+                int tot = 10 * 2016;
+                scale_bt<<<(tot + 255) / 256, 256, 0, stream>>>(W4, rsb, btS3, 2000,
+                                                                10, 2016);
+                fold_bias<<<1, 256, 0, stream>>>(W4, meanb, rsb, biasS, 2000, 10);
+            }
+            launch_gemm(2, nullptr, bufC, nullptr, btS3, 2000, 10, 2016, biasS,
+                        nullptr, bufB, 2048, 10, 0);
+            spmm_small_bf<<<N_NODES, 256, 0, stream>>>(bufB, row_ptr, cols_s,
+                                                       vals_s, bufC, 10, 10);
+            bn_zero(10);
+            col_stats<<<dim3(1, 200), 256, 0, stream>>>(bufC, ssum, ssq, 10, 100,
+                                                        10);
+            int tot = N_NODES * 10;
+            bn_elem_bf<<<(tot + 255) / 256, 256, 0, stream>>>(
+                bufC, ssum, ssq, brs[b].final_dest, 10, tot);
         }
     }
 
```

Result: slower. 6.089 ms (+7.0%).
